# Kernel optimization log

Hardware: AMD Instinct MI355X
Metric: run time of the kernel (lower is better)

Reference implementation:

```python
import jax, jax.numpy as jnp
import numpy as np

EPS = 1e-5  # torch LayerNorm default
N_BLOCKS = 8
N_NODES = 4096
BATCH = 4096


def setup_inputs() -> dict:
    key = jax.random.key(0)
    ks = jax.random.split(key, 4)
    scale = 1.0 / np.sqrt(N_NODES)  # keep activations sane through 8 GEMMs
    x = jax.random.normal(ks[0], (BATCH, N_NODES), dtype=jnp.float32)
    W = jax.random.normal(ks[1], (N_BLOCKS, N_NODES, N_NODES), dtype=jnp.float32) * scale
    b = jax.random.normal(ks[2], (N_BLOCKS, N_NODES), dtype=jnp.float32) * 0.01
    slope = jax.random.uniform(ks[3], (N_BLOCKS, N_NODES), dtype=jnp.float32)
    ln_g = jnp.ones((N_BLOCKS, N_NODES), dtype=jnp.float32)
    ln_b = jnp.zeros((N_BLOCKS, N_NODES), dtype=jnp.float32)
    return {"x": x, "ln_g": ln_g, "ln_b": ln_b, "W": W, "b": b, "slope": slope}


def _block(x, g, bt, Wi, bi, si):
    # LayerNorm over last dim (biased variance, eps inside sqrt) -> Linear -> per-feature LeakyReLU
    mu = jnp.mean(x, axis=-1, keepdims=True)
    var = jnp.mean(jnp.square(x - mu), axis=-1, keepdims=True)
    ln = (x - mu) * jax.lax.rsqrt(var + EPS) * g + bt
    y = jnp.einsum('bn,mn->bm', ln, Wi) + bi  # torch Linear: x @ W.T + b
    return jnp.where(y < 0, y * si, y)


def reference(x, ln_g, ln_b, W, b, slope):
    for i in range(N_BLOCKS):
        x = _block(x, ln_g[i], ln_b[i], W[i], b[i], slope[i])
    return x
```

## Files before the change

### kernel.cpp

```cpp
#include <hip/hip_runtime.h>
#include <hip/hip_bf16.h>

#define NNODES 4096
#define NBATCH 4096
#define NBLK 8
#define LN_EPS 1e-5f

typedef __attribute__((ext_vector_type(8))) short short8;
typedef __attribute__((ext_vector_type(4))) float f32x4;
typedef __attribute__((ext_vector_type(4))) unsigned short u16x4;
typedef unsigned short u16;

__device__ __forceinline__ u16 bf16_rn(float f) {
  unsigned int u = __builtin_bit_cast(unsigned int, f);
  u += 0x7fffu + ((u >> 16) & 1u);
  return (u16)(u >> 16);
}

__device__ __forceinline__ float bf16_to_f(u16 h) {
  unsigned int u = ((unsigned int)h) << 16;
  return __builtin_bit_cast(float, u);
}

__device__ __forceinline__ void load_lds16(const void* g, void* l) {
  __builtin_amdgcn_global_load_lds((const __attribute__((address_space(1))) void*)g,
                                   (__attribute__((address_space(3))) void*)l,
                                   16, 0, 0);
}

template <bool LNF32>
__global__ __launch_bounds__(256) void prep_kernel(const float* __restrict__ W,
                                                   u16* __restrict__ Wb,
                                                   const void* __restrict__ xin,
                                                   const float* __restrict__ g,
                                                   const float* __restrict__ bt,
                                                   u16* __restrict__ lnout) {
  __shared__ float sh[8];
  int t = threadIdx.x;
  if (blockIdx.x < 16384) {
    int idx = blockIdx.x * 256 + t;
    float4 v = ((const float4*)W)[idx];
    u16x4 o;
    o[0] = bf16_rn(v.x); o[1] = bf16_rn(v.y); o[2] = bf16_rn(v.z); o[3] = bf16_rn(v.w);
    ((u16x4*)Wb)[idx] = o;
    return;
  }
  int row = blockIdx.x - 16384;
  float f[16];
  float s = 0.f, ss = 0.f;
  if constexpr (LNF32) {
    const float4* xr = (const float4*)((const float*)xin + (size_t)row * NNODES);
#pragma unroll
    for (int q = 0; q < 4; ++q) {
      float4 v = xr[q * 256 + t];
      f[q * 4 + 0] = v.x; f[q * 4 + 1] = v.y; f[q * 4 + 2] = v.z; f[q * 4 + 3] = v.w;
      s  += v.x + v.y + v.z + v.w;
      ss += v.x * v.x + v.y * v.y + v.z * v.z + v.w * v.w;
    }
  } else {
    const u16* xr = (const u16*)xin + (size_t)row * NNODES;
#pragma unroll
    for (int q = 0; q < 2; ++q) {
      short8 v = *(const short8*)(xr + q * 2048 + t * 8);
#pragma unroll
      for (int j = 0; j < 8; ++j) {
        float fv = bf16_to_f((u16)v[j]);
        f[q * 8 + j] = fv;
        s += fv; ss += fv * fv;
      }
    }
  }
#pragma unroll
  for (int off = 32; off >= 1; off >>= 1) {
    s  += __shfl_xor(s, off, 64);
    ss += __shfl_xor(ss, off, 64);
  }
  int wid = t >> 6, lane = t & 63;
  if (lane == 0) { sh[wid] = s; sh[wid + 4] = ss; }
  __syncthreads();
  s  = sh[0] + sh[1] + sh[2] + sh[3];
  ss = sh[4] + sh[5] + sh[6] + sh[7];
  float mu  = s * (1.f / NNODES);
  float var = ss * (1.f / NNODES) - mu * mu;
  float rs  = rsqrtf(var + LN_EPS);
  if constexpr (LNF32) {
    u16x4* o = (u16x4*)(lnout + (size_t)row * NNODES);
    const float4* gv = (const float4*)g;
    const float4* bv = (const float4*)bt;
#pragma unroll
    for (int q = 0; q < 4; ++q) {
      int i = q * 256 + t;
      float4 gg = gv[i], bb = bv[i];
      u16x4 ov;
      ov[0] = bf16_rn((f[q * 4 + 0] - mu) * rs * gg.x + bb.x);
      ov[1] = bf16_rn((f[q * 4 + 1] - mu) * rs * gg.y + bb.y);
      ov[2] = bf16_rn((f[q * 4 + 2] - mu) * rs * gg.z + bb.z);
      ov[3] = bf16_rn((f[q * 4 + 3] - mu) * rs * gg.w + bb.w);
      o[i] = ov;
    }
  } else {
#pragma unroll
    for (int q = 0; q < 2; ++q) {
      int base = q * 2048 + t * 8;
      float4 g0 = ((const float4*)g)[base / 4], g1 = ((const float4*)g)[base / 4 + 1];
      float4 b0 = ((const float4*)bt)[base / 4], b1 = ((const float4*)bt)[base / 4 + 1];
      short8 sv;
      sv[0] = (short)bf16_rn((f[q * 8 + 0] - mu) * rs * g0.x + b0.x);
      sv[1] = (short)bf16_rn((f[q * 8 + 1] - mu) * rs * g0.y + b0.y);
      sv[2] = (short)bf16_rn((f[q * 8 + 2] - mu) * rs * g0.z + b0.z);
      sv[3] = (short)bf16_rn((f[q * 8 + 3] - mu) * rs * g0.w + b0.w);
      sv[4] = (short)bf16_rn((f[q * 8 + 4] - mu) * rs * g1.x + b1.x);
      sv[5] = (short)bf16_rn((f[q * 8 + 5] - mu) * rs * g1.y + b1.y);
      sv[6] = (short)bf16_rn((f[q * 8 + 6] - mu) * rs * g1.z + b1.z);
      sv[7] = (short)bf16_rn((f[q * 8 + 7] - mu) * rs * g1.w + b1.w);
      *(short8*)(lnout + (size_t)row * NNODES + base) = sv;
    }
  }
}


#define VMC(N) asm volatile("s_waitcnt vmcnt(" #N ")" ::: "memory")

#define STAGE_A(T, H)                                                          \
  { load_lds16(Asrc0 + (size_t)((H) * 128) * Kdim + (T) * 64,                  \
               ldsA + ((T) & 1) * 16384 + (H) * 8192 + tid * 8);               \
    load_lds16(Asrc0 + (size_t)((H) * 128 + 64) * Kdim + (T) * 64,             \
               ldsA + ((T) & 1) * 16384 + (H) * 8192 + 4096 + tid * 8); }

#define STAGE_B(T, H)                                                          \
  { load_lds16(Bsrc0 + (size_t)((H) * 128) * Kdim + (T) * 64,                  \
               ldsB + ((T) & 1) * 16384 + (H) * 8192 + tid * 8);               \
    load_lds16(Bsrc0 + (size_t)((H) * 128 + 64) * Kdim + (T) * 64,             \
               ldsB + ((T) & 1) * 16384 + (H) * 8192 + 4096 + tid * 8); }

#define PH(KT, MH, NH, STAGE_STMT, VM_STMT)                                    \
  {                                                                            \
    const u16* Ab = ldsA + ((KT) & 1) * 16384 + aBase + (MH) * 4096;           \
    const u16* Bb = ldsB + ((KT) & 1) * 16384 + bBase + (NH) * 2048;           \
    if ((NH) == 0) {                                                           \
      _Pragma("unroll") for (int mi = 0; mi < 4; ++mi) {                       \
        afr[mi][0] = *(const short8*)(Ab + mi * 1024 + gk0);                   \
        afr[mi][1] = *(const short8*)(Ab + mi * 1024 + gk1);                   \
      }                                                                        \
    }                                                                          \
    if ((MH) == 0) {                                                           \
      _Pragma("unroll") for (int ni = 0; ni < 2; ++ni) {                       \
        bfr[NH][ni][0] = *(const short8*)(Bb + ni * 1024 + gk0);               \
        bfr[NH][ni][1] = *(const short8*)(Bb + ni * 1024 + gk1);               \
      }                                                                        \
    }                                                                          \
    STAGE_STMT;                                                                \
    if ((NH) == 0 && (MH) == 0)                                                \
      asm volatile("s_waitcnt lgkmcnt(8)" ::: "memory");                       \
    VM_STMT;                                                                   \
    __builtin_amdgcn_s_barrier();                                              \
    asm volatile("s_waitcnt lgkmcnt(0)" ::: "memory");                         \
    __builtin_amdgcn_sched_barrier(0);                                         \
    __builtin_amdgcn_s_setprio(1);                                             \
    _Pragma("unroll") for (int mi = 0; mi < 4; ++mi)                           \
      _Pragma("unroll") for (int ni = 0; ni < 2; ++ni) {                       \
        acc[(MH) * 4 + mi][(NH) * 2 + ni] =                                    \
          __builtin_amdgcn_mfma_f32_16x16x32_bf16(afr[mi][0], bfr[NH][ni][0],  \
            acc[(MH) * 4 + mi][(NH) * 2 + ni], 0, 0, 0);                       \
        acc[(MH) * 4 + mi][(NH) * 2 + ni] =                                    \
          __builtin_amdgcn_mfma_f32_16x16x32_bf16(afr[mi][1], bfr[NH][ni][1],  \
            acc[(MH) * 4 + mi][(NH) * 2 + ni], 0, 0, 0);                       \
      }                                                                        \
    __builtin_amdgcn_s_setprio(0);                                             \
    __builtin_amdgcn_s_barrier();                                              \
  }

template <bool OUTF32>
__global__ __launch_bounds__(512, 2) void gemm256_kernel(const u16* __restrict__ A,
                                                         const u16* __restrict__ B,
                                                         const float* __restrict__ bias,
                                                         const float* __restrict__ slope,
                                                         void* __restrict__ Cv) {
  constexpr int Kdim = NNODES;
  __shared__ u16 lds[65536];
  u16* ldsA = lds;
  u16* ldsB = lds + 32768;

  const int tid  = threadIdx.x;
  const int lane = tid & 63;
  const int wid  = tid >> 6;
  const int wr   = wid >> 2;
  const int wc   = wid & 3;

  int bid = blockIdx.x;
  int swz = (bid & 7) * 32 + (bid >> 3);
  const int brow = (swz >> 4) * 256;
  const int bcol = (swz & 15) * 256;

  const int srow = tid >> 3;
  const int sg   = ((tid & 7) ^ (srow & 7)) * 8;
  const u16* Asrc0 = A + (size_t)(brow + srow) * Kdim + sg;
  const u16* Bsrc0 = B + (size_t)(bcol + srow) * Kdim + sg;

  const int r16 = lane & 15, kq = lane >> 4;
  const int g0  = kq ^ (r16 & 7);
  const int gk0 = g0 * 8, gk1 = (g0 ^ 4) * 8;
  const int aBase = wr * 8192 + r16 * 64;
  const int bBase = (wc >> 1) * 8192 + ((wc & 1) * 64 + r16) * 64;

  f32x4 acc[8][4] = {};
  short8 afr[4][2], bfr[2][2][2];

  STAGE_B(0, 0) STAGE_B(0, 1) STAGE_A(0, 0) STAGE_A(0, 1) STAGE_B(1, 0) STAGE_B(1, 1)
  VMC(4);
  __builtin_amdgcn_s_barrier();

  for (int t = 0; t < 31; ++t) {
    const int T = 2 * t;
    PH(T,     0, 0, STAGE_A(T + 1, 0), ;)
    PH(T,     0, 1, STAGE_A(T + 1, 1), ;)
    PH(T,     1, 0, STAGE_B(T + 2, 0), ;)
    PH(T,     1, 1, STAGE_B(T + 2, 1), VMC(4))
    PH(T + 1, 0, 0, STAGE_A(T + 2, 0), ;)
    PH(T + 1, 0, 1, STAGE_A(T + 2, 1), ;)
    PH(T + 1, 1, 0, STAGE_B(T + 3, 0), ;)
    PH(T + 1, 1, 1, STAGE_B(T + 3, 1), VMC(4))
  }
  PH(62, 0, 0, STAGE_A(63, 0), ;)
  PH(62, 0, 1, STAGE_A(63, 1), ;)
  PH(62, 1, 0, ;, ;)
  PH(62, 1, 1, ;, VMC(0))
  PH(63, 0, 0, ;, ;)
  PH(63, 0, 1, ;, ;)
  PH(63, 1, 0, ;, ;)
  PH(63, 1, 1, ;, ;)

  const int crow0 = brow + wr * 128 + (lane >> 4) * 4;
  const int ccol0 = bcol + wc * 64 + r16;
#pragma unroll
  for (int n = 0; n < 4; ++n) {
    int col = ccol0 + n * 16;
    float bv = bias[col], sv = slope[col];
#pragma unroll
    for (int m = 0; m < 8; ++m) {
      int row0 = crow0 + m * 16;
#pragma unroll
      for (int r = 0; r < 4; ++r) {
        float vv = acc[m][n][r] + bv;
        vv = vv < 0.f ? vv * sv : vv;
        if constexpr (OUTF32) {
          ((float*)Cv)[(size_t)(row0 + r) * NNODES + col] = vv;
        } else {
          ((u16*)Cv)[(size_t)(row0 + r) * NNODES + col] = bf16_rn(vv);
        }
      }
    }
  }
}

extern "C" void kernel_launch(void* const* d_in, const int* in_sizes, int n_in,
                              void* d_out, int out_size, void* d_ws, size_t ws_size,
                              hipStream_t stream) {
  const float* x     = (const float*)d_in[0];
  const float* ln_g  = (const float*)d_in[1];
  const float* ln_b  = (const float*)d_in[2];
  const float* W     = (const float*)d_in[3];
  const float* b     = (const float*)d_in[4];
  const float* slope = (const float*)d_in[5];
  float* out = (float*)d_out;

  char* ws = (char*)d_ws;
  u16* Wbuf  = (u16*)ws;
  u16* lnbuf = (u16*)(ws + (size_t)32 * 1024 * 1024);
  u16* ybuf  = (u16*)(ws + (size_t)64 * 1024 * 1024);

  const size_t WN = (size_t)NNODES * NNODES;
  const dim3 pgrid(16384 + NBATCH);

  for (int i = 0; i < NBLK; ++i) {
    if (i == 0)
      prep_kernel<true><<<pgrid, dim3(256), 0, stream>>>(W, Wbuf, (const void*)x,
                                                         ln_g, ln_b, lnbuf);
    else
      prep_kernel<false><<<pgrid, dim3(256), 0, stream>>>(W + WN * i, Wbuf, (const void*)ybuf,
                                                          ln_g + (size_t)i * NNODES,
                                                          ln_b + (size_t)i * NNODES, lnbuf);
    if (i == NBLK - 1)
      gemm256_kernel<true><<<dim3(256), dim3(512), 0, stream>>>(lnbuf, Wbuf,
                                                                b + (size_t)i * NNODES,
                                                                slope + (size_t)i * NNODES, (void*)out);
    else
      gemm256_kernel<false><<<dim3(256), dim3(512), 0, stream>>>(lnbuf, Wbuf,
                                                                 b + (size_t)i * NNODES,
                                                                 slope + (size_t)i * NNODES, (void*)ybuf);
  }
}
```

Before: 1.119 ms.

## Overlap next layer's weight bf16 conversion with the current GEMM main loop

The fp32-to-bf16 conversion of the next block's weight matrix moves into the GEMM kernel's K-loop, with the W buffer double-buffered. For layers after the first, the separate prep pass now only does LayerNorm, in a new dedicated kernel. The goal is to hide the standalone conversion pass, which is bandwidth-heavy, behind MFMA-bound GEMM work. In exchange, the extra global loads and stores share vmcnt waits with the LDS staging pipeline and may stall it, and they add registers.

New measurement: 1.095 ms. 2.2% less time.

```diff
diff --git a/kernel.cpp b/kernel.cpp
--- a/kernel.cpp
+++ b/kernel.cpp
@@ -48,27 +48,13 @@
   int row = blockIdx.x - 16384;
   float f[16];
   float s = 0.f, ss = 0.f;
-  if constexpr (LNF32) {
-    const float4* xr = (const float4*)((const float*)xin + (size_t)row * NNODES);
-#pragma unroll
-    for (int q = 0; q < 4; ++q) {
-      float4 v = xr[q * 256 + t];
-      f[q * 4 + 0] = v.x; f[q * 4 + 1] = v.y; f[q * 4 + 2] = v.z; f[q * 4 + 3] = v.w;
-      s  += v.x + v.y + v.z + v.w;
-      ss += v.x * v.x + v.y * v.y + v.z * v.z + v.w * v.w;
-    }
-  } else {
-    const u16* xr = (const u16*)xin + (size_t)row * NNODES;
-#pragma unroll
-    for (int q = 0; q < 2; ++q) {
-      short8 v = *(const short8*)(xr + q * 2048 + t * 8);
-#pragma unroll
-      for (int j = 0; j < 8; ++j) {
-        float fv = bf16_to_f((u16)v[j]);
-        f[q * 8 + j] = fv;
-        s += fv; ss += fv * fv;
-      }
-    }
+  const float4* xr = (const float4*)((const float*)xin + (size_t)row * NNODES);
+#pragma unroll
+  for (int q = 0; q < 4; ++q) {
+    float4 v = xr[q * 256 + t];
+    f[q * 4 + 0] = v.x; f[q * 4 + 1] = v.y; f[q * 4 + 2] = v.z; f[q * 4 + 3] = v.w;
+    s  += v.x + v.y + v.z + v.w;
+    ss += v.x * v.x + v.y * v.y + v.z * v.z + v.w * v.w;
   }
 #pragma unroll
   for (int off = 32; off >= 1; off >>= 1) {
@@ -83,38 +69,72 @@
   float mu  = s * (1.f / NNODES);
   float var = ss * (1.f / NNODES) - mu * mu;
   float rs  = rsqrtf(var + LN_EPS);
-  if constexpr (LNF32) {
-    u16x4* o = (u16x4*)(lnout + (size_t)row * NNODES);
-    const float4* gv = (const float4*)g;
-    const float4* bv = (const float4*)bt;
-#pragma unroll
-    for (int q = 0; q < 4; ++q) {
-      int i = q * 256 + t;
-      float4 gg = gv[i], bb = bv[i];
-      u16x4 ov;
-      ov[0] = bf16_rn((f[q * 4 + 0] - mu) * rs * gg.x + bb.x);
-      ov[1] = bf16_rn((f[q * 4 + 1] - mu) * rs * gg.y + bb.y);
-      ov[2] = bf16_rn((f[q * 4 + 2] - mu) * rs * gg.z + bb.z);
-      ov[3] = bf16_rn((f[q * 4 + 3] - mu) * rs * gg.w + bb.w);
-      o[i] = ov;
+  u16x4* o = (u16x4*)(lnout + (size_t)row * NNODES);
+  const float4* gv = (const float4*)g;
+  const float4* bv = (const float4*)bt;
+#pragma unroll
+  for (int q = 0; q < 4; ++q) {
+    int i = q * 256 + t;
+    float4 gg = gv[i], bb = bv[i];
+    u16x4 ov;
+    ov[0] = bf16_rn((f[q * 4 + 0] - mu) * rs * gg.x + bb.x);
+    ov[1] = bf16_rn((f[q * 4 + 1] - mu) * rs * gg.y + bb.y);
+    ov[2] = bf16_rn((f[q * 4 + 2] - mu) * rs * gg.z + bb.z);
+    ov[3] = bf16_rn((f[q * 4 + 3] - mu) * rs * gg.w + bb.w);
+    o[i] = ov;
+  }
+}
+
+__global__ __launch_bounds__(256) void ln_bf16_kernel(const u16* __restrict__ x,
+                                                      const float* __restrict__ g,
+                                                      const float* __restrict__ bt,
+                                                      u16* __restrict__ out) {
+  int row = blockIdx.x;
+  int t = threadIdx.x;
+  const u16* xr = x + (size_t)row * NNODES;
+  float f[2][8];
+  float s = 0.f, ss = 0.f;
+#pragma unroll
+  for (int q = 0; q < 2; ++q) {
+    short8 v = *(const short8*)(xr + q * 2048 + t * 8);
+#pragma unroll
+    for (int j = 0; j < 8; ++j) {
+      float fv = bf16_to_f((u16)v[j]);
+      f[q][j] = fv;
+      s += fv; ss += fv * fv;
     }
-  } else {
-#pragma unroll
-    for (int q = 0; q < 2; ++q) {
-      int base = q * 2048 + t * 8;
-      float4 g0 = ((const float4*)g)[base / 4], g1 = ((const float4*)g)[base / 4 + 1];
-      float4 b0 = ((const float4*)bt)[base / 4], b1 = ((const float4*)bt)[base / 4 + 1];
-      short8 sv;
-      sv[0] = (short)bf16_rn((f[q * 8 + 0] - mu) * rs * g0.x + b0.x);
-      sv[1] = (short)bf16_rn((f[q * 8 + 1] - mu) * rs * g0.y + b0.y);
-      sv[2] = (short)bf16_rn((f[q * 8 + 2] - mu) * rs * g0.z + b0.z);
-      sv[3] = (short)bf16_rn((f[q * 8 + 3] - mu) * rs * g0.w + b0.w);
-      sv[4] = (short)bf16_rn((f[q * 8 + 4] - mu) * rs * g1.x + b1.x);
-      sv[5] = (short)bf16_rn((f[q * 8 + 5] - mu) * rs * g1.y + b1.y);
-      sv[6] = (short)bf16_rn((f[q * 8 + 6] - mu) * rs * g1.z + b1.z);
-      sv[7] = (short)bf16_rn((f[q * 8 + 7] - mu) * rs * g1.w + b1.w);
-      *(short8*)(lnout + (size_t)row * NNODES + base) = sv;
-    }
+  }
+#pragma unroll
+  for (int off = 32; off >= 1; off >>= 1) {
+    s  += __shfl_xor(s, off, 64);
+    ss += __shfl_xor(ss, off, 64);
+  }
+  __shared__ float sh[8];
+  int wid = t >> 6, lane = t & 63;
+  if (lane == 0) { sh[wid] = s; sh[wid + 4] = ss; }
+  __syncthreads();
+  s  = sh[0] + sh[1] + sh[2] + sh[3];
+  ss = sh[4] + sh[5] + sh[6] + sh[7];
+  float mu  = s * (1.f / NNODES);
+  float var = ss * (1.f / NNODES) - mu * mu;
+  float rs  = rsqrtf(var + LN_EPS);
+  const float4* gv = (const float4*)g;
+  const float4* bv = (const float4*)bt;
+#pragma unroll
+  for (int q = 0; q < 2; ++q) {
+    int base = q * 2048 + t * 8;
+    float4 g0 = gv[base / 4], g1 = gv[base / 4 + 1];
+    float4 b0 = bv[base / 4], b1 = bv[base / 4 + 1];
+    short8 sv;
+    sv[0] = (short)bf16_rn((f[q][0] - mu) * rs * g0.x + b0.x);
+    sv[1] = (short)bf16_rn((f[q][1] - mu) * rs * g0.y + b0.y);
+    sv[2] = (short)bf16_rn((f[q][2] - mu) * rs * g0.z + b0.z);
+    sv[3] = (short)bf16_rn((f[q][3] - mu) * rs * g0.w + b0.w);
+    sv[4] = (short)bf16_rn((f[q][4] - mu) * rs * g1.x + b1.x);
+    sv[5] = (short)bf16_rn((f[q][5] - mu) * rs * g1.y + b1.y);
+    sv[6] = (short)bf16_rn((f[q][6] - mu) * rs * g1.z + b1.z);
+    sv[7] = (short)bf16_rn((f[q][7] - mu) * rs * g1.w + b1.w);
+    *(short8*)(out + (size_t)row * NNODES + base) = sv;
   }
 }
 
@@ -132,6 +152,31 @@
                ldsB + ((T) & 1) * 16384 + (H) * 8192 + tid * 8);               \
     load_lds16(Bsrc0 + (size_t)((H) * 128 + 64) * Kdim + (T) * 64,             \
                ldsB + ((T) & 1) * 16384 + (H) * 8192 + 4096 + tid * 8); }
+
+#define CVSTORE(SRC, CIDX)                                                     \
+  { __builtin_amdgcn_sched_barrier(0);                                         \
+    u16x4 o_;                                                                  \
+    o_[0] = bf16_rn(SRC[0]); o_[1] = bf16_rn(SRC[1]);                          \
+    o_[2] = bf16_rn(SRC[2]); o_[3] = bf16_rn(SRC[3]);                          \
+    *(u16x4*)(Wnd + cvoff + (size_t)(CIDX) * 2048) = o_; }
+
+#define CONVP3                                                                 \
+  { if (CONVON && t < 16) {                                                    \
+      const float* cp_ = Wns + cvoff + (size_t)(2 * t) * 2048;                 \
+      asm volatile("global_load_dwordx4 %0, %1, off"                           \
+                   : "=&v"(cvA) : "v"(cp_) : "memory");                        \
+    }                                                                          \
+    VMC(4);                                                                    \
+    if (CONVON && t >= 1 && t <= 16) CVSTORE(cvB, 2 * t - 1) }
+
+#define CONVP7                                                                 \
+  { if (CONVON && t < 16) {                                                    \
+      const float* cp_ = Wns + cvoff + (size_t)(2 * t + 1) * 2048;             \
+      asm volatile("global_load_dwordx4 %0, %1, off"                           \
+                   : "=&v"(cvB) : "v"(cp_) : "memory");                        \
+    }                                                                          \
+    VMC(4);                                                                    \
+    if (CONVON && t < 16) CVSTORE(cvA, 2 * t) }
 
 #define PH(KT, MH, NH, STAGE_STMT, VM_STMT)                                    \
   {                                                                            \
@@ -170,12 +215,14 @@
     __builtin_amdgcn_s_barrier();                                              \
   }
 
-template <bool OUTF32>
+template <bool OUTF32, bool CONVON>
 __global__ __launch_bounds__(512, 2) void gemm256_kernel(const u16* __restrict__ A,
                                                          const u16* __restrict__ B,
                                                          const float* __restrict__ bias,
                                                          const float* __restrict__ slope,
-                                                         void* __restrict__ Cv) {
+                                                         void* __restrict__ Cv,
+                                                         const float* __restrict__ Wns,
+                                                         u16* __restrict__ Wnd) {
   constexpr int Kdim = NNODES;
   __shared__ u16 lds[65536];
   u16* ldsA = lds;
@@ -203,6 +250,9 @@
   const int aBase = wr * 8192 + r16 * 64;
   const int bBase = (wc >> 1) * 8192 + ((wc & 1) * 64 + r16) * 64;
 
+  const size_t cvoff = (size_t)bid * 65536 + tid * 4;
+  f32x4 cvA, cvB;
+
   f32x4 acc[8][4] = {};
   short8 afr[4][2], bfr[2][2][2];
 
@@ -215,11 +265,11 @@
     PH(T,     0, 0, STAGE_A(T + 1, 0), ;)
     PH(T,     0, 1, STAGE_A(T + 1, 1), ;)
     PH(T,     1, 0, STAGE_B(T + 2, 0), ;)
-    PH(T,     1, 1, STAGE_B(T + 2, 1), VMC(4))
+    PH(T,     1, 1, STAGE_B(T + 2, 1), CONVP3)
     PH(T + 1, 0, 0, STAGE_A(T + 2, 0), ;)
     PH(T + 1, 0, 1, STAGE_A(T + 2, 1), ;)
     PH(T + 1, 1, 0, STAGE_B(T + 3, 0), ;)
-    PH(T + 1, 1, 1, STAGE_B(T + 3, 1), VMC(4))
+    PH(T + 1, 1, 1, STAGE_B(T + 3, 1), CONVP7)
   }
   PH(62, 0, 0, STAGE_A(63, 0), ;)
   PH(62, 0, 1, STAGE_A(63, 1), ;)
@@ -265,28 +315,30 @@
   float* out = (float*)d_out;
 
   char* ws = (char*)d_ws;
-  u16* Wbuf  = (u16*)ws;
-  u16* lnbuf = (u16*)(ws + (size_t)32 * 1024 * 1024);
-  u16* ybuf  = (u16*)(ws + (size_t)64 * 1024 * 1024);
+  u16* Wbuf0 = (u16*)ws;
+  u16* Wbuf1 = (u16*)(ws + (size_t)32 * 1024 * 1024);
+  u16* lnbuf = (u16*)(ws + (size_t)64 * 1024 * 1024);
+  u16* ybuf  = (u16*)(ws + (size_t)96 * 1024 * 1024);
 
   const size_t WN = (size_t)NNODES * NNODES;
-  const dim3 pgrid(16384 + NBATCH);
 
   for (int i = 0; i < NBLK; ++i) {
+    u16* Wc = (i & 1) ? Wbuf1 : Wbuf0;
+    u16* Wn = (i & 1) ? Wbuf0 : Wbuf1;
     if (i == 0)
-      prep_kernel<true><<<pgrid, dim3(256), 0, stream>>>(W, Wbuf, (const void*)x,
-                                                         ln_g, ln_b, lnbuf);
+      prep_kernel<true><<<dim3(16384 + NBATCH), dim3(256), 0, stream>>>(
+          W, Wbuf0, (const void*)x, ln_g, ln_b, lnbuf);
     else
-      prep_kernel<false><<<pgrid, dim3(256), 0, stream>>>(W + WN * i, Wbuf, (const void*)ybuf,
-                                                          ln_g + (size_t)i * NNODES,
-                                                          ln_b + (size_t)i * NNODES, lnbuf);
+      ln_bf16_kernel<<<dim3(NBATCH), dim3(256), 0, stream>>>(
+          ybuf, ln_g + (size_t)i * NNODES, ln_b + (size_t)i * NNODES, lnbuf);
+
     if (i == NBLK - 1)
-      gemm256_kernel<true><<<dim3(256), dim3(512), 0, stream>>>(lnbuf, Wbuf,
-                                                                b + (size_t)i * NNODES,
-                                                                slope + (size_t)i * NNODES, (void*)out);
+      gemm256_kernel<true, false><<<dim3(256), dim3(512), 0, stream>>>(
+          lnbuf, Wc, b + (size_t)i * NNODES, slope + (size_t)i * NNODES,
+          (void*)out, nullptr, nullptr);
     else
-      gemm256_kernel<false><<<dim3(256), dim3(512), 0, stream>>>(lnbuf, Wbuf,
-                                                                 b + (size_t)i * NNODES,
-                                                                 slope + (size_t)i * NNODES, (void*)ybuf);
-  }
-}
+      gemm256_kernel<false, true><<<dim3(256), dim3(512), 0, stream>>>(
+          lnbuf, Wc, b + (size_t)i * NNODES, slope + (size_t)i * NNODES,
+          (void*)ybuf, W + WN * (i + 1), Wn);
+  }
+}
```
